# Kernel optimization log

Measured on AMD Instinct MI355X. Metric: run time of the kernel, lower is better.

## Reference

```python
import jax, jax.numpy as jnp
import numpy as np

B, IN, H = 4096, 1024, 2048


def setup_inputs() -> dict:
    key = jax.random.key(0)
    k1, k2, k3, k4 = jax.random.split(key, 4)
    x = jax.random.normal(k1, (B, IN), dtype=jnp.float32)
    h_prev = jax.random.normal(k2, (B, H), dtype=jnp.float32)
    c_prev = jax.random.normal(k3, (B, H), dtype=jnp.float32)
    # Fused weight for the 5 gate Linears (Wf, Wi, Wc, Wo, We), columns stacked.
    # Scaled like PyTorch Linear default init (~uniform(-1/sqrt(fan_in))).
    W = jax.random.normal(k4, (IN + H, 5 * H), dtype=jnp.float32) / jnp.sqrt(jnp.float32(IN + H))
    b = jnp.zeros((5 * H,), dtype=jnp.float32)
    return {"x": x, "h_prev": h_prev, "c_prev": c_prev, "W": W, "b": b}


def reference(x, h_prev, c_prev, W, b):
    combined = jnp.concatenate([x, h_prev], axis=1)          # [B, IN+H]
    z = combined @ W + b                                      # [B, 5H] single fused GEMM
    f, i, c_hat, o, e = jnp.split(z, 5, axis=1)
    ft = jax.nn.sigmoid(f)
    it = jax.nn.sigmoid(i)
    ct_hat = jnp.tanh(c_hat)
    ot = jax.nn.sigmoid(o)
    et = jax.nn.sigmoid(e)
    ct = ft * c_prev + it * ct_hat
    ht = ot * jnp.tanh(ct)
    ht = et * jnp.exp(ht) + (1.0 - et) * ht
    return ht, ct
```

## Files before the change

### kernel.cpp

```cpp
#include <hip/hip_runtime.h>
#include <hip/hip_bf16.h>
#include <stdint.h>

#define B_  4096
#define IN_ 1024
#define H_  2048
#define K_  (IN_ + H_)
#define N_  (5 * H_)

#define BM2 256
#define BJ2 32
#define BK2 64
#define NT2 48

typedef __attribute__((ext_vector_type(8))) short   short8;
typedef __attribute__((ext_vector_type(4))) float   f32x4;
typedef __attribute__((ext_vector_type(8))) unsigned short ushort8;

__device__ __forceinline__ unsigned short f2bf(float f) {
  union { float f; unsigned u; } cv; cv.f = f;
  unsigned u = cv.u;
  u += 0x7fffu + ((u >> 16) & 1u);
  return (unsigned short)(u >> 16);
}

__device__ __forceinline__ void async16(const unsigned short* g, unsigned short* l) {
  __builtin_amdgcn_global_load_lds(
      (const __attribute__((address_space(1))) unsigned int*)g,
      (__attribute__((address_space(3))) unsigned int*)(void*)l,
      16, 0, 0);
}

__device__ __forceinline__ float fsig(float x) {
  return __builtin_amdgcn_rcpf(1.f + __expf(-x));
}
__device__ __forceinline__ float ftanh(float x) {
  return 1.f - 2.f * __builtin_amdgcn_rcpf(__expf(2.f * x) + 1.f);
}

__global__ void build_combined(const float* __restrict__ x,
                               const float* __restrict__ h,
                               unsigned short* __restrict__ out) {
  const int row = blockIdx.x;
  const float4* xr = (const float4*)(x + (size_t)row * IN_);
  const float4* hr = (const float4*)(h + (size_t)row * H_);
  uint2* orow = (uint2*)(out + (size_t)row * K_);
  for (int c = threadIdx.x; c < K_ / 4; c += 256) {
    float4 v = (c < IN_ / 4) ? xr[c] : hr[c - IN_ / 4];
    uint2 p;
    p.x = (unsigned)f2bf(v.x) | ((unsigned)f2bf(v.y) << 16);
    p.y = (unsigned)f2bf(v.z) | ((unsigned)f2bf(v.w) << 16);
    orow[c] = p;
  }
}

__global__ __launch_bounds__(256) void transpose_convert(
    const float* __restrict__ W, unsigned short* __restrict__ Wt) {
  __shared__ float tile[64][65];
  const int n0 = blockIdx.x * 64;
  const int k0 = blockIdx.y * 64;
  const int t  = threadIdx.x;

  const int r0 = t >> 4;
  const int c4 = t & 15;
  #pragma unroll
  for (int i = 0; i < 4; ++i) {
    const int kk = i * 16 + r0;
    const float4 v = *(const float4*)&W[(size_t)(k0 + kk) * N_ + n0 + c4 * 4];
    float* dst = &tile[kk][c4 * 4];
    dst[0] = v.x; dst[1] = v.y; dst[2] = v.z; dst[3] = v.w;
  }
  __syncthreads();

  #pragma unroll
  for (int i = 0; i < 2; ++i) {
    const int c2 = t + i * 256;
    const int nn = c2 >> 3;
    const int kc = (c2 & 7) * 8;
    ushort8 p;
    #pragma unroll
    for (int u = 0; u < 8; ++u) p[u] = f2bf(tile[kc + u][nn]);
    *(ushort8*)&Wt[(size_t)(n0 + nn) * K_ + k0 + kc] = p;
  }
}

__global__ __launch_bounds__(512, 2) void gemm_fused(
    const unsigned short* __restrict__ A,
    const unsigned short* __restrict__ Bt,
    const float* __restrict__ c_prev,
    const float* __restrict__ bias,
    float* __restrict__ out)
{
  __shared__ unsigned short As[2][BM2 * BK2];
  __shared__ unsigned short Bs[2][5 * BJ2 * BK2];

  const int tid  = threadIdx.x;
  const int wave = tid >> 6;
  const int lane = tid & 63;
  const int quad = lane >> 4;
  const int lr   = lane & 15;

  const int tile_m = blockIdx.x >> 6;
  const int tile_j = blockIdx.x & 63;
  const int m0 = tile_m * BM2;
  const int j0 = tile_j * BJ2;

  const int wm = (wave & 3) * 64;
  const int wn = (wave >> 2) * 16;

  f32x4 acc[4][5];
  #pragma unroll
  for (int mi = 0; mi < 4; ++mi)
    #pragma unroll
    for (int g = 0; g < 5; ++g)
      acc[mi][g] = (f32x4){0.f, 0.f, 0.f, 0.f};

  const int lrow8 = lane >> 3;
  const int sw8   = ((lane & 7) ^ lrow8) * 8;

  const unsigned short* aSrc =
      A + (size_t)(m0 + 8 * wave + lrow8) * K_ + sw8;

  const bool doTail = (wave < 4);
  const int cB0 = wave;
  const int cB1 = wave + 8;
  const int cB2 = doTail ? wave + 16 : wave;
  const unsigned short* bSrc0 =
      Bt + (size_t)((cB0 >> 2) * H_ + j0 + (cB0 & 3) * 8 + lrow8) * K_ + sw8;
  const unsigned short* bSrc1 =
      Bt + (size_t)((cB1 >> 2) * H_ + j0 + (cB1 & 3) * 8 + lrow8) * K_ + sw8;
  const unsigned short* bSrc2 =
      Bt + (size_t)((cB2 >> 2) * H_ + j0 + (cB2 & 3) * 8 + lrow8) * K_ + sw8;

  #define STAGE_A(ko_, bb) do {                                        \
    async16(aSrc + (ko_),                    &As[bb][512 * wave]);     \
    async16(aSrc + (size_t) 64 * K_ + (ko_), &As[bb][512 * (wave + 8)]);  \
    async16(aSrc + (size_t)128 * K_ + (ko_), &As[bb][512 * (wave + 16)]); \
    async16(aSrc + (size_t)192 * K_ + (ko_), &As[bb][512 * (wave + 24)]); \
  } while (0)
  #define STAGE_B(ko_, bb) do {                                        \
    async16(bSrc0 + (ko_), &Bs[bb][512 * cB0]);                        \
    async16(bSrc1 + (ko_), &Bs[bb][512 * cB1]);                        \
    if (doTail) async16(bSrc2 + (ko_), &Bs[bb][512 * cB2]);            \
  } while (0)

  STAGE_A((size_t)0, 0);
  STAGE_B((size_t)0, 0);

  const int rs0 = ((0 + quad) ^ (lr & 7)) * 8;
  const int rs1 = ((4 + quad) ^ (lr & 7)) * 8;
  const int aR[4] = { (wm + 0 * 16 + lr) * BK2, (wm + 1 * 16 + lr) * BK2,
                      (wm + 2 * 16 + lr) * BK2, (wm + 3 * 16 + lr) * BK2 };
  const int bR[5] = { (0 * 32 + wn + lr) * BK2, (1 * 32 + wn + lr) * BK2,
                      (2 * 32 + wn + lr) * BK2, (3 * 32 + wn + lr) * BK2,
                      (4 * 32 + wn + lr) * BK2 };

  #pragma unroll 2
  for (int t = 0; t < NT2; ++t) {
    const int cur = t & 1;
    const size_t koN = (size_t)(t + 1) * BK2;

    if (t < NT2 - 1) STAGE_A(koN, cur ^ 1);
    if (t == NT2 - 1) asm volatile("s_waitcnt vmcnt(0)" ::: "memory");
    else              asm volatile("s_waitcnt vmcnt(4)" ::: "memory");
    __builtin_amdgcn_s_barrier();

    short8 af0[4], bf0[5];
    #pragma unroll
    for (int mi = 0; mi < 4; ++mi)
      af0[mi] = *(const short8*)&As[cur][aR[mi] + rs0];
    #pragma unroll
    for (int g = 0; g < 5; ++g)
      bf0[g] = *(const short8*)&Bs[cur][bR[g] + rs0];
    asm volatile("s_waitcnt lgkmcnt(0)" ::: "memory");
    __builtin_amdgcn_sched_barrier(0);

    __builtin_amdgcn_s_setprio(1);
    #pragma unroll
    for (int mi = 0; mi < 4; ++mi)
      #pragma unroll
      for (int g = 0; g < 5; ++g)
        acc[mi][g] = __builtin_amdgcn_mfma_f32_16x16x32_bf16(
            af0[mi], bf0[g], acc[mi][g], 0, 0, 0);
    __builtin_amdgcn_s_setprio(0);
    __builtin_amdgcn_s_barrier();

    if (t < NT2 - 1) STAGE_B(koN, cur ^ 1);
    short8 af1[4], bf1[5];
    #pragma unroll
    for (int mi = 0; mi < 4; ++mi)
      af1[mi] = *(const short8*)&As[cur][aR[mi] + rs1];
    #pragma unroll
    for (int g = 0; g < 5; ++g)
      bf1[g] = *(const short8*)&Bs[cur][bR[g] + rs1];
    __builtin_amdgcn_s_barrier();
    asm volatile("s_waitcnt lgkmcnt(0)" ::: "memory");
    __builtin_amdgcn_sched_barrier(0);

    __builtin_amdgcn_s_setprio(1);
    #pragma unroll
    for (int mi = 0; mi < 4; ++mi)
      #pragma unroll
      for (int g = 0; g < 5; ++g)
        acc[mi][g] = __builtin_amdgcn_mfma_f32_16x16x32_bf16(
            af1[mi], bf1[g], acc[mi][g], 0, 0, 0);
    __builtin_amdgcn_s_setprio(0);
    __builtin_amdgcn_s_barrier();
  }
  #undef STAGE_A
  #undef STAGE_B

  const int col = j0 + wn + lr;
  float bb[5];
  #pragma unroll
  for (int g = 0; g < 5; ++g) bb[g] = bias[g * H_ + col];

  #pragma unroll
  for (int mi = 0; mi < 4; ++mi) {
    const int rbase = m0 + wm + mi * 16 + quad * 4;
    float cp[4];
    #pragma unroll
    for (int r = 0; r < 4; ++r)
      cp[r] = c_prev[(size_t)(rbase + r) * H_ + col];
    #pragma unroll
    for (int r = 0; r < 4; ++r) {
      const float ft = fsig(acc[mi][0][r] + bb[0]);
      const float it = fsig(acc[mi][1][r] + bb[1]);
      const float ch = ftanh(acc[mi][2][r] + bb[2]);
      const float ot = fsig(acc[mi][3][r] + bb[3]);
      const float et = fsig(acc[mi][4][r] + bb[4]);
      const float ct = ft * cp[r] + it * ch;
      const float th = ftanh(ct);
      float ht = ot * th;
      ht = et * __expf(ht) + (1.f - et) * ht;
      out[(size_t)(rbase + r) * H_ + col] = ht;
      out[(size_t)B_ * H_ + (size_t)(rbase + r) * H_ + col] = ct;
    }
  }
}

extern "C" void kernel_launch(void* const* d_in, const int* in_sizes, int n_in,
                              void* d_out, int out_size, void* d_ws, size_t ws_size,
                              hipStream_t stream) {
  const float* x = (const float*)d_in[0];
  const float* h = (const float*)d_in[1];
  const float* c = (const float*)d_in[2];
  const float* W = (const float*)d_in[3];
  const float* b = (const float*)d_in[4];
  float* out = (float*)d_out;

  char* ws = (char*)d_ws;
  unsigned short* combined = (unsigned short*)ws;
  unsigned short* Wt = (unsigned short*)(ws + (size_t)25165824);

  build_combined<<<B_, 256, 0, stream>>>(x, h, combined);
  transpose_convert<<<dim3(N_ / 64, K_ / 64), 256, 0, stream>>>(W, Wt);
  gemm_fused<<<(B_ / BM2) * (H_ / BJ2), 512, 0, stream>>>(combined, Wt, c, b, out);
}
```

Before: 539.1 us.

## Double GEMM block N-tile and merge A/B staging with fewer barriers

Widens each block's hidden-column tile from 32 to 64 per gate, so a wave now computes a 128x80 output region with 8x5 MFMA accumulators. A and B prefetch are merged into one async stage per iteration, and two of the per-iteration barriers are removed. The aim is more reuse of each loaded A and B fragment and less synchronisation per k-step. The cost is a much larger register and LDS footprint (about 144KB LDS and 160 accumulator registers per thread) under an unchanged launch_bounds(512,2). That likely lowers occupancy to one block per CU and may cause register spills.

```diff
diff --git a/kernel.cpp b/kernel.cpp
--- a/kernel.cpp
+++ b/kernel.cpp
@@ -9,7 +9,7 @@
 #define N_  (5 * H_)
 
 #define BM2 256
-#define BJ2 32
+#define BJ2 64
 #define BK2 64
 #define NT2 48
 
@@ -100,17 +100,17 @@
   const int quad = lane >> 4;
   const int lr   = lane & 15;
 
-  const int tile_m = blockIdx.x >> 6;
-  const int tile_j = blockIdx.x & 63;
+  const int tile_m = blockIdx.x >> 5;
+  const int tile_j = blockIdx.x & 31;
   const int m0 = tile_m * BM2;
   const int j0 = tile_j * BJ2;
 
-  const int wm = (wave & 3) * 64;
-  const int wn = (wave >> 2) * 16;
-
-  f32x4 acc[4][5];
-  #pragma unroll
-  for (int mi = 0; mi < 4; ++mi)
+  const int wm  = (wave & 1) * 128;
+  const int wnq = (wave >> 1) * 16;
+
+  f32x4 acc[8][5];
+  #pragma unroll
+  for (int mi = 0; mi < 8; ++mi)
     #pragma unroll
     for (int g = 0; g < 5; ++g)
       acc[mi][g] = (f32x4){0.f, 0.f, 0.f, 0.f};
@@ -118,56 +118,45 @@
   const int lrow8 = lane >> 3;
   const int sw8   = ((lane & 7) ^ lrow8) * 8;
 
-  const unsigned short* aSrc =
+  const unsigned short* aS0 =
       A + (size_t)(m0 + 8 * wave + lrow8) * K_ + sw8;
-
-  const bool doTail = (wave < 4);
-  const int cB0 = wave;
-  const int cB1 = wave + 8;
-  const int cB2 = doTail ? wave + 16 : wave;
-  const unsigned short* bSrc0 =
-      Bt + (size_t)((cB0 >> 2) * H_ + j0 + (cB0 & 3) * 8 + lrow8) * K_ + sw8;
-  const unsigned short* bSrc1 =
-      Bt + (size_t)((cB1 >> 2) * H_ + j0 + (cB1 & 3) * 8 + lrow8) * K_ + sw8;
-  const unsigned short* bSrc2 =
-      Bt + (size_t)((cB2 >> 2) * H_ + j0 + (cB2 & 3) * 8 + lrow8) * K_ + sw8;
-
-  #define STAGE_A(ko_, bb) do {                                        \
-    async16(aSrc + (ko_),                    &As[bb][512 * wave]);     \
-    async16(aSrc + (size_t) 64 * K_ + (ko_), &As[bb][512 * (wave + 8)]);  \
-    async16(aSrc + (size_t)128 * K_ + (ko_), &As[bb][512 * (wave + 16)]); \
-    async16(aSrc + (size_t)192 * K_ + (ko_), &As[bb][512 * (wave + 24)]); \
+  const unsigned short* bS0 =
+      Bt + (size_t)(j0 + 8 * wave + lrow8) * K_ + sw8;
+
+  #define STAGE(ko_, bb) do {                                            \
+    async16(aS0 + (ko_),                       &As[bb][512 * wave]);     \
+    async16(aS0 + (size_t) 64 * K_ + (ko_),    &As[bb][512 * (wave + 8)]);  \
+    async16(aS0 + (size_t)128 * K_ + (ko_),    &As[bb][512 * (wave + 16)]); \
+    async16(aS0 + (size_t)192 * K_ + (ko_),    &As[bb][512 * (wave + 24)]); \
+    async16(bS0 + (ko_),                       &Bs[bb][512 * wave]);     \
+    async16(bS0 + (size_t)(1 * H_) * K_ + (ko_), &Bs[bb][512 * (wave + 8)]);  \
+    async16(bS0 + (size_t)(2 * H_) * K_ + (ko_), &Bs[bb][512 * (wave + 16)]); \
+    async16(bS0 + (size_t)(3 * H_) * K_ + (ko_), &Bs[bb][512 * (wave + 24)]); \
+    async16(bS0 + (size_t)(4 * H_) * K_ + (ko_), &Bs[bb][512 * (wave + 32)]); \
   } while (0)
-  #define STAGE_B(ko_, bb) do {                                        \
-    async16(bSrc0 + (ko_), &Bs[bb][512 * cB0]);                        \
-    async16(bSrc1 + (ko_), &Bs[bb][512 * cB1]);                        \
-    if (doTail) async16(bSrc2 + (ko_), &Bs[bb][512 * cB2]);            \
-  } while (0)
-
-  STAGE_A((size_t)0, 0);
-  STAGE_B((size_t)0, 0);
+
+  STAGE((size_t)0, 0);
 
   const int rs0 = ((0 + quad) ^ (lr & 7)) * 8;
   const int rs1 = ((4 + quad) ^ (lr & 7)) * 8;
-  const int aR[4] = { (wm + 0 * 16 + lr) * BK2, (wm + 1 * 16 + lr) * BK2,
-                      (wm + 2 * 16 + lr) * BK2, (wm + 3 * 16 + lr) * BK2 };
-  const int bR[5] = { (0 * 32 + wn + lr) * BK2, (1 * 32 + wn + lr) * BK2,
-                      (2 * 32 + wn + lr) * BK2, (3 * 32 + wn + lr) * BK2,
-                      (4 * 32 + wn + lr) * BK2 };
+  int aR[8], bR[5];
+  #pragma unroll
+  for (int mi = 0; mi < 8; ++mi) aR[mi] = (wm + mi * 16 + lr) * BK2;
+  #pragma unroll
+  for (int g = 0; g < 5; ++g)    bR[g]  = (g * 64 + wnq + lr) * BK2;
 
   #pragma unroll 2
   for (int t = 0; t < NT2; ++t) {
     const int cur = t & 1;
-    const size_t koN = (size_t)(t + 1) * BK2;
-
-    if (t < NT2 - 1) STAGE_A(koN, cur ^ 1);
+
+    if (t < NT2 - 1) STAGE((size_t)(t + 1) * BK2, cur ^ 1);
     if (t == NT2 - 1) asm volatile("s_waitcnt vmcnt(0)" ::: "memory");
-    else              asm volatile("s_waitcnt vmcnt(4)" ::: "memory");
+    else              asm volatile("s_waitcnt vmcnt(9)" ::: "memory");
     __builtin_amdgcn_s_barrier();
 
-    short8 af0[4], bf0[5];
-    #pragma unroll
-    for (int mi = 0; mi < 4; ++mi)
+    short8 af0[8], bf0[5];
+    #pragma unroll
+    for (int mi = 0; mi < 8; ++mi)
       af0[mi] = *(const short8*)&As[cur][aR[mi] + rs0];
     #pragma unroll
     for (int g = 0; g < 5; ++g)
@@ -177,46 +166,43 @@
 
     __builtin_amdgcn_s_setprio(1);
     #pragma unroll
-    for (int mi = 0; mi < 4; ++mi)
+    for (int mi = 0; mi < 8; ++mi)
       #pragma unroll
       for (int g = 0; g < 5; ++g)
         acc[mi][g] = __builtin_amdgcn_mfma_f32_16x16x32_bf16(
             af0[mi], bf0[g], acc[mi][g], 0, 0, 0);
     __builtin_amdgcn_s_setprio(0);
-    __builtin_amdgcn_s_barrier();
-
-    if (t < NT2 - 1) STAGE_B(koN, cur ^ 1);
-    short8 af1[4], bf1[5];
-    #pragma unroll
-    for (int mi = 0; mi < 4; ++mi)
+    __builtin_amdgcn_sched_barrier(0);
+
+    short8 af1[8], bf1[5];
+    #pragma unroll
+    for (int mi = 0; mi < 8; ++mi)
       af1[mi] = *(const short8*)&As[cur][aR[mi] + rs1];
     #pragma unroll
     for (int g = 0; g < 5; ++g)
       bf1[g] = *(const short8*)&Bs[cur][bR[g] + rs1];
-    __builtin_amdgcn_s_barrier();
     asm volatile("s_waitcnt lgkmcnt(0)" ::: "memory");
     __builtin_amdgcn_sched_barrier(0);
+    __builtin_amdgcn_s_barrier();
 
     __builtin_amdgcn_s_setprio(1);
     #pragma unroll
-    for (int mi = 0; mi < 4; ++mi)
+    for (int mi = 0; mi < 8; ++mi)
       #pragma unroll
       for (int g = 0; g < 5; ++g)
         acc[mi][g] = __builtin_amdgcn_mfma_f32_16x16x32_bf16(
             af1[mi], bf1[g], acc[mi][g], 0, 0, 0);
     __builtin_amdgcn_s_setprio(0);
-    __builtin_amdgcn_s_barrier();
-  }
-  #undef STAGE_A
-  #undef STAGE_B
-
-  const int col = j0 + wn + lr;
+  }
+  #undef STAGE
+
+  const int col = j0 + wnq + lr;
   float bb[5];
   #pragma unroll
   for (int g = 0; g < 5; ++g) bb[g] = bias[g * H_ + col];
 
   #pragma unroll
-  for (int mi = 0; mi < 4; ++mi) {
+  for (int mi = 0; mi < 8; ++mi) {
     const int rbase = m0 + wm + mi * 16 + quad * 4;
     float cp[4];
     #pragma unroll
```

Result: slower. 848.6 us (+57.4%).
